# Optimization experiments

Measured on AMD Instinct MI355X. Metric: run time of the kernel, lower is better.

Reference implementation:

```python
import math
import jax, jax.numpy as jnp
import numpy as np

N, E, H, D, NNZ = 32768, 512, 8, 64, 524288


def setup_inputs() -> dict:
    key = jax.random.key(0)
    ks = jax.random.split(key, 12)
    x = jax.random.normal(ks[0], (N, E), dtype=jnp.float32)
    row_index = jnp.sort(jax.random.randint(ks[1], (NNZ,), 0, N))
    col_index = jax.random.randint(ks[2], (NNZ,), 0, N)
    to_col_index = jax.random.randint(ks[3], (N,), 0, N)
    att_bias = jax.random.normal(ks[4], (H, NNZ), dtype=jnp.float32)
    # positive interatomic distances in ~[0.5, 5.5)
    dist = jax.random.uniform(ks[5], (NNZ,), dtype=jnp.float32) * 5.0 + 0.5
    pos = jax.random.normal(ks[6], (N, 3), dtype=jnp.float32)
    col_pos = jax.random.normal(ks[7], (N, 3), dtype=jnp.float32)
    s = 1.0 / math.sqrt(E)
    q_w = jax.random.normal(ks[8], (E, E), dtype=jnp.float32) * s
    q_b = jax.random.normal(ks[9], (E,), dtype=jnp.float32) * 0.02
    k_w = jax.random.normal(ks[10], (E, E), dtype=jnp.float32) * s
    k_b = jax.random.normal(ks[11], (E,), dtype=jnp.float32) * 0.02
    return {"x": x, "row_index": row_index, "col_index": col_index,
            "to_col_index": to_col_index, "att_bias": att_bias, "dist": dist,
            "pos": pos, "col_pos": col_pos,
            "q_w": q_w, "q_b": q_b, "k_w": k_w, "k_b": k_b}


def reference(x, row_index, col_index, to_col_index, att_bias, dist, pos, col_pos,
              q_w, q_b, k_w, k_b):
    n = x.shape[0]
    h = att_bias.shape[0]
    d = x.shape[1] // h
    # per-head projections: [N, H, D]
    q = (x @ q_w.T + q_b).reshape(n, h, d) * (1.0 / math.sqrt(d))
    k = (x @ k_w.T + k_b).reshape(n, h, d)[to_col_index]  # [Nk, H, D]
    # sparse (COO) masked q @ k^T plus additive bias -> per-edge logits [nnz, H]
    logits = jnp.einsum('ehd,ehd->eh', q[row_index], k[col_index]) + att_bias.T
    # sparse softmax over each query row (per head)
    m = jax.ops.segment_max(logits, row_index, num_segments=n)       # [N, H]
    p = jnp.exp(logits - m[row_index])
    z = jax.ops.segment_sum(p, row_index, num_segments=n)            # [N, H]
    att = p / z[row_index]                                           # [nnz, H]
    # distance-weighted attention (dist==0 -> contribution 0, as x/inf in torch)
    inv_d = jnp.where(dist == 0, 0.0, 1.0 / dist)
    att = att * inv_d[:, None]
    # sparse bmm against col_pos values and against ones
    cp = col_pos[col_index]                                          # [nnz, 3]
    dst_vec = jax.ops.segment_sum(att[:, :, None] * cp[:, None, :],
                                  row_index, num_segments=n)         # [N, H, 3]
    avg_inv_dist = jax.ops.segment_sum(att, row_index, num_segments=n)  # [N, H]
    src_vec = avg_inv_dist[..., None] * pos[:, None, :]              # [N, H, 3]
    v = dst_vec - src_vec
    norm = jnp.sqrt(jnp.sum(v * v, axis=-1, keepdims=True))
    feat3 = v / jnp.maximum(norm, 1e-12)                             # F.normalize
    feat = jnp.concatenate([feat3, avg_inv_dist[..., None]], axis=-1)  # [N, H, 4]
    return feat.reshape(n, h * 4)
```

## Files before the change

### kernel.cpp

```cpp
#include <hip/hip_runtime.h>
#include <math.h>
#include <stdint.h>

#define N_NODES 32768
#define E_DIM   512
#define H_HEADS 8
#define D_HEAD  64
#define NNZ_E   524288

typedef __attribute__((ext_vector_type(4))) float f32x4;
typedef __attribute__((ext_vector_type(8))) _Float16 f16x8;

__device__ __forceinline__ void async16(const void* g, void* l) {
  __builtin_amdgcn_global_load_lds(
      (const __attribute__((address_space(1))) void*)g,
      (__attribute__((address_space(3))) void*)l, 16, 0, 0);
}

__device__ __forceinline__ float dot8(const f16x8 a, const f16x8 b, float acc) {
#if __has_builtin(__builtin_amdgcn_fdot2)
  acc = __builtin_amdgcn_fdot2(__builtin_shufflevector(a, a, 0, 1),
                               __builtin_shufflevector(b, b, 0, 1), acc, false);
  acc = __builtin_amdgcn_fdot2(__builtin_shufflevector(a, a, 2, 3),
                               __builtin_shufflevector(b, b, 2, 3), acc, false);
  acc = __builtin_amdgcn_fdot2(__builtin_shufflevector(a, a, 4, 5),
                               __builtin_shufflevector(b, b, 4, 5), acc, false);
  acc = __builtin_amdgcn_fdot2(__builtin_shufflevector(a, a, 6, 7),
                               __builtin_shufflevector(b, b, 6, 7), acc, false);
#else
#pragma unroll
  for (int i = 0; i < 8; ++i) acc = fmaf((float)a[i], (float)b[i], acc);
#endif
  return acc;
}

__global__ __launch_bounds__(256) void prep_small(
    const float* __restrict__ q_w, const float* __restrict__ k_w,
    const int* __restrict__ row_index, const int* __restrict__ col_index,
    const int* __restrict__ to_col,
    _Float16* __restrict__ wq_h, _Float16* __restrict__ wk_h,
    int* __restrict__ row_start, int* __restrict__ ge) {
  const int b = blockIdx.x;
  if (b < 256) {
    const float* src = (b < 128) ? q_w : k_w;
    _Float16* dst = (b < 128) ? wq_h : wk_h;
    const int t = (b & 127) * 256 + threadIdx.x;
    const int r = t >> 6;
    const int c8 = (t & 63) << 3;
    const float4 v0 = *(const float4*)(src + (size_t)r * 512 + c8);
    const float4 v1 = *(const float4*)(src + (size_t)r * 512 + c8 + 4);
    f16x8 o;
    o[0] = (_Float16)v0.x; o[1] = (_Float16)v0.y;
    o[2] = (_Float16)v0.z; o[3] = (_Float16)v0.w;
    o[4] = (_Float16)v1.x; o[5] = (_Float16)v1.y;
    o[6] = (_Float16)v1.z; o[7] = (_Float16)v1.w;
    *(f16x8*)(dst + (size_t)r * 512 + c8) = o;
  } else {
    const int e = (b - 256) * 256 + threadIdx.x;
    if (e < NNZ_E) {
      ge[e] = to_col[col_index[e]];
      const int r0 = row_index[e];
      const int r1 = (e + 1 < NNZ_E) ? row_index[e + 1] : N_NODES;
      if (e == 0)
        for (int r = 0; r <= r0; ++r) row_start[r] = 0;
      for (int r = r0 + 1; r <= r1; ++r) row_start[r] = e + 1;
    }
  }
}

__global__ __launch_bounds__(256) void gemm_mfma(
    const float* __restrict__ x,
    const _Float16* __restrict__ wqh,
    const _Float16* __restrict__ wkh,
    const float* __restrict__ q_b, const float* __restrict__ k_b,
    _Float16* __restrict__ qh, _Float16* __restrict__ kh) {
  __shared__ float Af[128 * 32];
  __shared__ _Float16 Bh[128 * 32];
  const int tid = threadIdx.x;
  const int w = tid >> 6;
  const int l = tid & 63;

  const int b = blockIdx.x;
  const int j = b >> 3;
  const int mb = (b & 7) * 32 + (j >> 3);
  const int c = j & 7;
  const bool is_q = ((c & 1) == 0);
  const int bm = mb * 128;
  const int bn = (c >> 1) * 128;

  const _Float16* __restrict__ wmat = is_q ? wqh : wkh;
  const float* __restrict__ bias = is_q ? q_b : k_b;
  _Float16* __restrict__ outp = is_q ? qh : kh;
  const float oscale = is_q ? 0.125f : 1.0f;

  const int wm = (w & 1) * 64;
  const int wn = (w >> 1) * 64;

  f32x4 acc[4][4];
#pragma unroll
  for (int i = 0; i < 4; ++i)
#pragma unroll
    for (int jj = 0; jj < 4; ++jj) acc[i][jj] = (f32x4){0.f, 0.f, 0.f, 0.f};

  const int ar = l >> 3;
  const int agc = (l & 7) ^ ar;
  const int sr0 = w * 16 + (l >> 2);
  const int sr1 = sr0 + 64;
  const int sc = (((l & 3) ^ ((l >> 3) & 3)) << 3);
  const int fr = l & 15;
  const int fcs = ((((l >> 4) ^ ((fr >> 1) & 3)) & 3) << 3);
  const int akc = (l >> 4) * 2;
  const int as = l & 7;

  const _Float16* __restrict__ wa = wmat + (size_t)bn * 512;

  for (int k0 = 0; k0 < 512; k0 += 32) {
#pragma unroll
    for (int cc = 0; cc < 4; ++cc) {
      const int rbase = cc * 32 + w * 8;
      async16(x + (size_t)(bm + rbase + ar) * 512 + k0 + agc * 4,
              Af + rbase * 32);
    }
    async16(wa + (size_t)sr0 * 512 + k0 + sc, Bh + w * 512);
    async16(wa + (size_t)sr1 * 512 + k0 + sc, Bh + (w + 4) * 512);
    __syncthreads();

    f16x8 av[4], bv[4];
#pragma unroll
    for (int i = 0; i < 4; ++i) {
      const float* rp = Af + (wm + i * 16 + fr) * 32;
      const float4 fa = *(const float4*)(rp + ((akc ^ as) << 2));
      const float4 fb = *(const float4*)(rp + (((akc + 1) ^ as) << 2));
      f16x8 v;
      v[0] = (_Float16)fa.x; v[1] = (_Float16)fa.y;
      v[2] = (_Float16)fa.z; v[3] = (_Float16)fa.w;
      v[4] = (_Float16)fb.x; v[5] = (_Float16)fb.y;
      v[6] = (_Float16)fb.z; v[7] = (_Float16)fb.w;
      av[i] = v;
    }
#pragma unroll
    for (int i = 0; i < 4; ++i)
      bv[i] = *(const f16x8*)(Bh + (wn + i * 16 + fr) * 32 + fcs);
#pragma unroll
    for (int i = 0; i < 4; ++i)
#pragma unroll
      for (int jj = 0; jj < 4; ++jj)
        acc[i][jj] = __builtin_amdgcn_mfma_f32_16x16x32_f16(
            av[i], bv[jj], acc[i][jj], 0, 0, 0);
    __syncthreads();
  }

  const int cn = l & 15;
  const int cm4 = (l >> 4) * 4;
  float bvals[4];
#pragma unroll
  for (int jj = 0; jj < 4; ++jj) bvals[jj] = bias[bn + wn + jj * 16 + cn];
#pragma unroll
  for (int i = 0; i < 4; ++i) {
#pragma unroll
    for (int r = 0; r < 4; ++r) {
      const int m = bm + wm + i * 16 + cm4 + r;
      _Float16* op = outp + (size_t)m * 512 + bn + wn + cn;
#pragma unroll
      for (int jj = 0; jj < 4; ++jj) {
        op[jj * 16] = (_Float16)((acc[i][jj][r] + bvals[jj]) * oscale);
      }
    }
  }
}

__global__ __launch_bounds__(256) void row_fused(
    const _Float16* __restrict__ qh, const _Float16* __restrict__ kh,
    const int* __restrict__ row_start, const int* __restrict__ ge,
    const float* __restrict__ att_bias, const int* __restrict__ col_index,
    const float* __restrict__ dist, const float* __restrict__ pos,
    const float* __restrict__ col_pos, float* __restrict__ out) {
  const int r = blockIdx.x * 4 + (threadIdx.x >> 6);
  const int lane = threadIdx.x & 63;
  const int h = lane >> 3;
  const int start = row_start[r];
  const int end = row_start[r + 1];

  const f16x8 qv = *(const f16x8*)(qh + (size_t)r * E_DIM + lane * 8);
  const float* __restrict__ biasp = att_bias + (size_t)h * NNZ_E;

  float m = -INFINITY, l = 0.f, accw = 0.f, a0 = 0.f, a1 = 0.f, a2 = 0.f;

  auto edge_logit = [&](const f16x8 kv) -> float {
    float s = dot8(qv, kv, 0.f);
    s += __shfl_xor(s, 1);
    s += __shfl_xor(s, 2);
    s += __shfl_xor(s, 4);
    return s;
  };
  auto upd = [&](float logit, float dd, float c0, float c1, float c2) {
    const float w = (dd == 0.f) ? 0.f : __builtin_amdgcn_rcpf(dd);
    const float nm = fmaxf(m, logit);
    const float sc = __expf(m - nm);
    const float p = __expf(logit - nm);
    m = nm;
    l = fmaf(l, sc, p);
    const float pw = p * w;
    accw = fmaf(accw, sc, pw);
    a0 = fmaf(a0, sc, pw * c0);
    a1 = fmaf(a1, sc, pw * c1);
    a2 = fmaf(a2, sc, pw * c2);
  };

  int e = start;
  for (; e + 4 <= end; e += 4) {
    int g[4], cc[4];
    float dd[4], bb[4], cp[4][3];
    f16x8 kv[4];
#pragma unroll
    for (int i = 0; i < 4; ++i) g[i] = ge[e + i];
#pragma unroll
    for (int i = 0; i < 4; ++i)
      kv[i] = *(const f16x8*)(kh + (size_t)g[i] * E_DIM + lane * 8);
#pragma unroll
    for (int i = 0; i < 4; ++i) {
      cc[i] = col_index[e + i];
      dd[i] = dist[e + i];
      bb[i] = biasp[e + i];
    }
#pragma unroll
    for (int i = 0; i < 4; ++i) {
      cp[i][0] = col_pos[cc[i] * 3 + 0];
      cp[i][1] = col_pos[cc[i] * 3 + 1];
      cp[i][2] = col_pos[cc[i] * 3 + 2];
    }
    float s[4];
#pragma unroll
    for (int i = 0; i < 4; ++i) s[i] = edge_logit(kv[i]) + bb[i];
#pragma unroll
    for (int i = 0; i < 4; ++i) upd(s[i], dd[i], cp[i][0], cp[i][1], cp[i][2]);
  }
  for (; e < end; ++e) {
    const int g0 = ge[e];
    const f16x8 kv0 = *(const f16x8*)(kh + (size_t)g0 * E_DIM + lane * 8);
    const int c0 = col_index[e];
    const float dd0 = dist[e];
    const float bb0 = biasp[e];
    const float cp00 = col_pos[c0 * 3 + 0];
    const float cp01 = col_pos[c0 * 3 + 1];
    const float cp02 = col_pos[c0 * 3 + 2];
    const float s0 = edge_logit(kv0) + bb0;
    upd(s0, dd0, cp00, cp01, cp02);
  }

  if ((lane & 7) == 0) {
    const float invz = (l > 0.f) ? 1.f / l : 0.f;
    const float avg = accw * invz;
    const float v0 = a0 * invz - avg * pos[r * 3 + 0];
    const float v1 = a1 * invz - avg * pos[r * 3 + 1];
    const float v2 = a2 * invz - avg * pos[r * 3 + 2];
    const float nrm = sqrtf(v0 * v0 + v1 * v1 + v2 * v2);
    const float invn = 1.f / fmaxf(nrm, 1e-12f);
    float4 o;
    o.x = v0 * invn; o.y = v1 * invn; o.z = v2 * invn; o.w = avg;
    *(float4*)(out + (size_t)r * (H_HEADS * 4) + h * 4) = o;
  }
}

extern "C" void kernel_launch(void* const* d_in, const int* in_sizes, int n_in,
                              void* d_out, int out_size, void* d_ws,
                              size_t ws_size, hipStream_t stream) {
  const float* x        = (const float*)d_in[0];
  const int* row_index  = (const int*)d_in[1];
  const int* col_index  = (const int*)d_in[2];
  const int* to_col     = (const int*)d_in[3];
  const float* att_bias = (const float*)d_in[4];
  const float* dist     = (const float*)d_in[5];
  const float* pos      = (const float*)d_in[6];
  const float* col_pos  = (const float*)d_in[7];
  const float* q_w      = (const float*)d_in[8];
  const float* q_b      = (const float*)d_in[9];
  const float* k_w      = (const float*)d_in[10];
  const float* k_b      = (const float*)d_in[11];
  float* out = (float*)d_out;

  _Float16* qh = (_Float16*)d_ws;
  _Float16* kh = qh + (size_t)N_NODES * 512;
  _Float16* wq_h = kh + (size_t)N_NODES * 512;
  _Float16* wk_h = wq_h + 512 * 512;
  int* row_start = (int*)(wk_h + 512 * 512);
  int* ge = row_start + (N_NODES + 1);

  prep_small<<<256 + NNZ_E / 256, 256, 0, stream>>>(
      q_w, k_w, row_index, col_index, to_col, wq_h, wk_h, row_start, ge);

  gemm_mfma<<<2048, 256, 0, stream>>>(x, wq_h, wk_h, q_b, k_b, qh, kh);

  row_fused<<<N_NODES / 4, 256, 0, stream>>>(qh, kh, row_start, ge, att_bias,
                                             col_index, dist, pos, col_pos,
                                             out);
}
```

Baseline: 283.3 us.

## Pre-convert x to fp16 and fold edge index prep into GEMM launch

Adds an fp16 copy of x produced in the prep kernel, so the GEMM loads A tiles as fp16 through async LDS copies instead of loading fp32 and converting per tile. Each of the 16 output tiles sharing an A tile previously reloaded 256 bytes per row, now 128, at the cost of an extra full pass that reads x and writes a 32 MB fp16 copy. The edge-index preparation (ge, row_start) moves into extra blocks of the GEMM launch.

```diff
diff --git a/kernel.cpp b/kernel.cpp
--- a/kernel.cpp
+++ b/kernel.cpp
@@ -35,28 +35,44 @@
 }
 
 __global__ __launch_bounds__(256) void prep_small(
+    const float* __restrict__ x,
     const float* __restrict__ q_w, const float* __restrict__ k_w,
+    _Float16* __restrict__ wq_h, _Float16* __restrict__ wk_h,
+    _Float16* __restrict__ xs) {
+  const int b = blockIdx.x;
+  const float* src;
+  _Float16* dst;
+  int t;
+  if (b < 128)      { src = q_w; dst = wq_h; t = b * 256 + threadIdx.x; }
+  else if (b < 256) { src = k_w; dst = wk_h; t = (b - 128) * 256 + threadIdx.x; }
+  else              { src = x;   dst = xs;   t = (b - 256) * 256 + threadIdx.x; }
+  const int r = t >> 6;
+  const int c8 = (t & 63) << 3;
+  const float4 v0 = *(const float4*)(src + (size_t)r * 512 + c8);
+  const float4 v1 = *(const float4*)(src + (size_t)r * 512 + c8 + 4);
+  f16x8 o;
+  o[0] = (_Float16)v0.x; o[1] = (_Float16)v0.y;
+  o[2] = (_Float16)v0.z; o[3] = (_Float16)v0.w;
+  o[4] = (_Float16)v1.x; o[5] = (_Float16)v1.y;
+  o[6] = (_Float16)v1.z; o[7] = (_Float16)v1.w;
+  *(f16x8*)(dst + (size_t)r * 512 + c8) = o;
+}
+
+__global__ __launch_bounds__(256) void gemm_mfma(
+    const _Float16* __restrict__ xs,
+    const _Float16* __restrict__ wqh,
+    const _Float16* __restrict__ wkh,
+    const float* __restrict__ q_b, const float* __restrict__ k_b,
+    _Float16* __restrict__ qh, _Float16* __restrict__ kh,
     const int* __restrict__ row_index, const int* __restrict__ col_index,
     const int* __restrict__ to_col,
-    _Float16* __restrict__ wq_h, _Float16* __restrict__ wk_h,
     int* __restrict__ row_start, int* __restrict__ ge) {
+  __shared__ _Float16 Ah[128 * 32];
+  __shared__ _Float16 Bh[128 * 32];
   const int b = blockIdx.x;
-  if (b < 256) {
-    const float* src = (b < 128) ? q_w : k_w;
-    _Float16* dst = (b < 128) ? wq_h : wk_h;
-    const int t = (b & 127) * 256 + threadIdx.x;
-    const int r = t >> 6;
-    const int c8 = (t & 63) << 3;
-    const float4 v0 = *(const float4*)(src + (size_t)r * 512 + c8);
-    const float4 v1 = *(const float4*)(src + (size_t)r * 512 + c8 + 4);
-    f16x8 o;
-    o[0] = (_Float16)v0.x; o[1] = (_Float16)v0.y;
-    o[2] = (_Float16)v0.z; o[3] = (_Float16)v0.w;
-    o[4] = (_Float16)v1.x; o[5] = (_Float16)v1.y;
-    o[6] = (_Float16)v1.z; o[7] = (_Float16)v1.w;
-    *(f16x8*)(dst + (size_t)r * 512 + c8) = o;
-  } else {
-    const int e = (b - 256) * 256 + threadIdx.x;
+
+  if (b >= 2048) {
+    const int e = (b - 2048) * 256 + threadIdx.x;
     if (e < NNZ_E) {
       ge[e] = to_col[col_index[e]];
       const int r0 = row_index[e];
@@ -65,22 +81,13 @@
         for (int r = 0; r <= r0; ++r) row_start[r] = 0;
       for (int r = r0 + 1; r <= r1; ++r) row_start[r] = e + 1;
     }
-  }
-}
-
-__global__ __launch_bounds__(256) void gemm_mfma(
-    const float* __restrict__ x,
-    const _Float16* __restrict__ wqh,
-    const _Float16* __restrict__ wkh,
-    const float* __restrict__ q_b, const float* __restrict__ k_b,
-    _Float16* __restrict__ qh, _Float16* __restrict__ kh) {
-  __shared__ float Af[128 * 32];
-  __shared__ _Float16 Bh[128 * 32];
+    return;
+  }
+
   const int tid = threadIdx.x;
   const int w = tid >> 6;
   const int l = tid & 63;
 
-  const int b = blockIdx.x;
   const int j = b >> 3;
   const int mb = (b & 7) * 32 + (j >> 3);
   const int c = j & 7;
@@ -102,42 +109,26 @@
 #pragma unroll
     for (int jj = 0; jj < 4; ++jj) acc[i][jj] = (f32x4){0.f, 0.f, 0.f, 0.f};
 
-  const int ar = l >> 3;
-  const int agc = (l & 7) ^ ar;
   const int sr0 = w * 16 + (l >> 2);
   const int sr1 = sr0 + 64;
   const int sc = (((l & 3) ^ ((l >> 3) & 3)) << 3);
   const int fr = l & 15;
   const int fcs = ((((l >> 4) ^ ((fr >> 1) & 3)) & 3) << 3);
-  const int akc = (l >> 4) * 2;
-  const int as = l & 7;
 
   const _Float16* __restrict__ wa = wmat + (size_t)bn * 512;
+  const _Float16* __restrict__ xa = xs + (size_t)bm * 512;
 
   for (int k0 = 0; k0 < 512; k0 += 32) {
-#pragma unroll
-    for (int cc = 0; cc < 4; ++cc) {
-      const int rbase = cc * 32 + w * 8;
-      async16(x + (size_t)(bm + rbase + ar) * 512 + k0 + agc * 4,
-              Af + rbase * 32);
-    }
+    async16(xa + (size_t)sr0 * 512 + k0 + sc, Ah + w * 512);
+    async16(xa + (size_t)sr1 * 512 + k0 + sc, Ah + (w + 4) * 512);
     async16(wa + (size_t)sr0 * 512 + k0 + sc, Bh + w * 512);
     async16(wa + (size_t)sr1 * 512 + k0 + sc, Bh + (w + 4) * 512);
     __syncthreads();
 
     f16x8 av[4], bv[4];
 #pragma unroll
-    for (int i = 0; i < 4; ++i) {
-      const float* rp = Af + (wm + i * 16 + fr) * 32;
-      const float4 fa = *(const float4*)(rp + ((akc ^ as) << 2));
-      const float4 fb = *(const float4*)(rp + (((akc + 1) ^ as) << 2));
-      f16x8 v;
-      v[0] = (_Float16)fa.x; v[1] = (_Float16)fa.y;
-      v[2] = (_Float16)fa.z; v[3] = (_Float16)fa.w;
-      v[4] = (_Float16)fb.x; v[5] = (_Float16)fb.y;
-      v[6] = (_Float16)fb.z; v[7] = (_Float16)fb.w;
-      av[i] = v;
-    }
+    for (int i = 0; i < 4; ++i)
+      av[i] = *(const f16x8*)(Ah + (wm + i * 16 + fr) * 32 + fcs);
 #pragma unroll
     for (int i = 0; i < 4; ++i)
       bv[i] = *(const f16x8*)(Bh + (wn + i * 16 + fr) * 32 + fcs);
@@ -281,15 +272,17 @@
 
   _Float16* qh = (_Float16*)d_ws;
   _Float16* kh = qh + (size_t)N_NODES * 512;
-  _Float16* wq_h = kh + (size_t)N_NODES * 512;
+  _Float16* xs = kh + (size_t)N_NODES * 512;
+  _Float16* wq_h = xs + (size_t)N_NODES * 512;
   _Float16* wk_h = wq_h + 512 * 512;
   int* row_start = (int*)(wk_h + 512 * 512);
   int* ge = row_start + (N_NODES + 1);
 
-  prep_small<<<256 + NNZ_E / 256, 256, 0, stream>>>(
-      q_w, k_w, row_index, col_index, to_col, wq_h, wk_h, row_start, ge);
-
-  gemm_mfma<<<2048, 256, 0, stream>>>(x, wq_h, wk_h, q_b, k_b, qh, kh);
+  prep_small<<<8448, 256, 0, stream>>>(x, q_w, k_w, wq_h, wk_h, xs);
+
+  gemm_mfma<<<4096, 256, 0, stream>>>(xs, wq_h, wk_h, q_b, k_b, qh, kh,
+                                      row_index, col_index, to_col,
+                                      row_start, ge);
 
   row_fused<<<N_NODES / 4, 256, 0, stream>>>(qh, kh, row_start, ge, att_bias,
                                              col_index, dist, pos, col_pos,
```

After: 268.3 us. 1.06x faster.
